# Kernel tuning notes

Measured on AMD Instinct MI355X. Metric: run time of the kernel, lower is better.

## Reference

```python
import jax, jax.numpy as jnp
import numpy as np

B, N, T, H = 32, 16, 64, 256


def setup_inputs() -> dict:
    key = jax.random.key(0)
    k1, k2, k3 = jax.random.split(key, 3)
    node_rnn_output = jax.random.normal(k1, (B, T, H), dtype=jnp.float32)
    neigh_rnn_output = jax.random.normal(k2, (B, N, T, H), dtype=jnp.float32)
    # neighbor counts in [1, N] to avoid divide-by-zero in 1/sqrt scaling
    neighbors_number = jax.random.randint(k3, (B,), 1, N + 1, dtype=jnp.int64)
    return {
        "node_rnn_output": node_rnn_output,
        "neigh_rnn_output": neigh_rnn_output,
        "neighbors_number": neighbors_number,
    }


def reference(node_rnn_output, neigh_rnn_output, neighbors_number):
    b, t, h = node_rnn_output.shape
    n = neigh_rnn_output.shape[1]
    # [B, N*T, H]
    flat_neigh = neigh_rnn_output.reshape(b, n * t, h)
    # repeat node output along time axis: [B, N*T, H]
    stacked_node = jnp.tile(node_rnn_output, (1, n, 1))
    # S = flat_neigh @ stacked_node^T : [B, N*T, N*T]
    S = jnp.einsum("bqh,bkh->bqk", flat_neigh, stacked_node)
    scale = jnp.sqrt(neighbors_number.astype(S.dtype))  # [B]
    S = S / scale[:, None, None]
    A = jax.nn.softmax(S, axis=-1)
    # dropout with p=0 (eval / reference) is identity
    W = A.sum(axis=1).reshape(b, n, t)  # [B, N, T]
    output = jnp.einsum("bqk,bkh->bqh", A, flat_neigh)  # [B, N*T, H]
    return (output, W)
```

## Files before the change

kernel.cpp:

```cpp
#include <hip/hip_runtime.h>

#define Bc  32
#define Nc  16
#define Tc  64
#define Hc  256
#define NTc 1024

typedef unsigned short u16;
using v8s = __attribute__((ext_vector_type(8))) short;
using v4f = __attribute__((ext_vector_type(4))) float;

static __device__ __forceinline__ u16 f2bf(float x) {
    unsigned u = __float_as_uint(x);
    unsigned r = u + 0x7fffu + ((u >> 16) & 1u);
    return (u16)(r >> 16);
}
static __device__ __forceinline__ float bf2f(u16 h) {
    return __uint_as_float(((unsigned)h) << 16);
}

__global__ __launch_bounds__(256) void prep_kernel(const float* __restrict__ neigh,
                                                   const float* __restrict__ node,
                                                   u16* __restrict__ MT,
                                                   u16* __restrict__ NH,
                                                   u16* __restrict__ NL,
                                                   float* __restrict__ Wsum) {
    __shared__ float Ls[64][68];
    int bk = blockIdx.x, tid = threadIdx.x;

    if (bk < 128) {
        int b = bk >> 2, h0 = (bk & 3) << 6;
#pragma unroll
        for (int rep = 0; rep < 4; rep++) {
            int idx = rep * 256 + tid;
            int t = idx >> 4, c4 = idx & 15;
            const float4* p = (const float4*)(neigh + ((size_t)b * Nc * Tc + t) * Hc + h0) + c4;
            float4 a = make_float4(0.f, 0.f, 0.f, 0.f);
#pragma unroll
            for (int i = 0; i < Nc; i++) {
                float4 v = p[(size_t)i * (Tc * Hc / 4)];
                a.x += v.x; a.y += v.y; a.z += v.z; a.w += v.w;
            }
            const float r = 1.0f / 16.0f;
            Ls[t][c4 * 4 + 0] = a.x * r;
            Ls[t][c4 * 4 + 1] = a.y * r;
            Ls[t][c4 * 4 + 2] = a.z * r;
            Ls[t][c4 * 4 + 3] = a.w * r;
        }
        __syncthreads();
#pragma unroll
        for (int rep = 0; rep < 4; rep++) {
            int idx = rep * 256 + tid;
            int h = idx >> 4, t4 = idx & 15;
            ushort4 o;
            o.x = f2bf(Ls[t4 * 4 + 0][h]);
            o.y = f2bf(Ls[t4 * 4 + 1][h]);
            o.z = f2bf(Ls[t4 * 4 + 2][h]);
            o.w = f2bf(Ls[t4 * 4 + 3][h]);
            *(ushort4*)(MT + ((size_t)b * Hc + h0 + h) * Tc + t4 * 4) = o;
        }
    } else {
        int b = bk - 128;
#pragma unroll
        for (int rep = 0; rep < 16; rep++) {
            int idx = rep * 256 + tid;
            int t = idx >> 6, c4 = idx & 63;
            size_t off = ((size_t)b * Tc + t) * Hc + c4 * 4;
            float4 v = *(const float4*)(node + off);
            ushort4 hs, ls;
            hs.x = f2bf(v.x); ls.x = f2bf(v.x - bf2f(hs.x));
            hs.y = f2bf(v.y); ls.y = f2bf(v.y - bf2f(hs.y));
            hs.z = f2bf(v.z); ls.z = f2bf(v.z - bf2f(hs.z));
            hs.w = f2bf(v.w); ls.w = f2bf(v.w - bf2f(hs.w));
            *(ushort4*)(NH + off) = hs;
            *(ushort4*)(NL + off) = ls;
        }
        if (tid < 64) Wsum[b * 64 + tid] = 0.f;
    }
}

__global__ __launch_bounds__(256, 2) void fused_kernel(const float* __restrict__ neigh,
                                                       const u16* __restrict__ NH,
                                                       const u16* __restrict__ NL,
                                                       const int* __restrict__ nbr,
                                                       const u16* __restrict__ MT,
                                                       float* __restrict__ out,
                                                       float* __restrict__ Wsum) {
    __shared__ u16 Ph[64][72];

    int b  = blockIdx.x >> 4;
    int i  = blockIdx.x & 15;
    int q0 = i << 6;

    int tid  = threadIdx.x;
    int w    = tid >> 6;
    int lane = tid & 63;
    int quad = lane >> 4;
    int c    = lane & 15;

    int nb = (nbr[1] == 0) ? nbr[2 * b] : nbr[b];
    float rscale = rsqrtf((float)nb);

    const float* Xg  = neigh + ((size_t)(b * Nc + i) * Tc + w * 16 + c) * Hc;
    const u16*   NHg = NH + (size_t)b * Tc * Hc;
    const u16*   NLg = NL + (size_t)b * Tc * Hc;
    const u16*   MTg = MT + (size_t)b * Hc * Tc;

    v4f acc[4];
#pragma unroll
    for (int nt = 0; nt < 4; nt++)
#pragma unroll
        for (int rg = 0; rg < 4; rg++) acc[nt][rg] = 0.f;

#pragma unroll 2
    for (int k0 = 0; k0 < Hc; k0 += 32) {
        const float4* xp = (const float4*)(Xg + k0) + quad * 2;
        float4 x0 = xp[0];
        float4 x1 = xp[1];
        float xs[8] = {x0.x, x0.y, x0.z, x0.w, x1.x, x1.y, x1.z, x1.w};
        v8s ah, al;
#pragma unroll
        for (int j = 0; j < 8; j++) {
            u16 h = f2bf(xs[j]);
            ah[j] = (short)h;
            al[j] = (short)f2bf(xs[j] - bf2f(h));
        }
        size_t koff = (size_t)k0 + quad * 8;
#pragma unroll
        for (int nt = 0; nt < 4; nt++) {
            size_t roff = (size_t)(nt * 16 + c) * Hc + koff;
            v8s bh = *(const v8s*)(NHg + roff);
            v8s bl = *(const v8s*)(NLg + roff);
            acc[nt] = __builtin_amdgcn_mfma_f32_16x16x32_bf16(ah, bh, acc[nt], 0, 0, 0);
            acc[nt] = __builtin_amdgcn_mfma_f32_16x16x32_bf16(ah, bl, acc[nt], 0, 0, 0);
            acc[nt] = __builtin_amdgcn_mfma_f32_16x16x32_bf16(al, bh, acc[nt], 0, 0, 0);
        }
    }

#pragma unroll
    for (int nt = 0; nt < 4; nt++)
#pragma unroll
        for (int rg = 0; rg < 4; rg++) acc[nt][rg] *= rscale;

#pragma unroll
    for (int rg = 0; rg < 4; rg++) {
        float m = fmaxf(fmaxf(acc[0][rg], acc[1][rg]), fmaxf(acc[2][rg], acc[3][rg]));
#pragma unroll
        for (int d = 1; d < 16; d <<= 1) m = fmaxf(m, __shfl_xor(m, d));
        float e0 = __expf(acc[0][rg] - m);
        float e1 = __expf(acc[1][rg] - m);
        float e2 = __expf(acc[2][rg] - m);
        float e3 = __expf(acc[3][rg] - m);
        float s = e0 + e1 + e2 + e3;
#pragma unroll
        for (int d = 1; d < 16; d <<= 1) s += __shfl_xor(s, d);
        float inv = 1.0f / s;
        acc[0][rg] = e0 * inv; acc[1][rg] = e1 * inv;
        acc[2][rg] = e2 * inv; acc[3][rg] = e3 * inv;
    }

#pragma unroll
    for (int nt = 0; nt < 4; nt++) {
        float cs = acc[nt][0] + acc[nt][1] + acc[nt][2] + acc[nt][3];
        cs += __shfl_xor(cs, 16);
        cs += __shfl_xor(cs, 32);
        if (quad == 0) atomicAdd(&Wsum[b * Tc + nt * 16 + c], cs);
    }

#pragma unroll
    for (int nt = 0; nt < 4; nt++)
#pragma unroll
        for (int rg = 0; rg < 4; rg++)
            Ph[w * 16 + quad * 4 + rg][nt * 16 + c] = f2bf(acc[nt][rg]);

    __syncthreads();

    v8s pa0 = *(const v8s*)&Ph[w * 16 + c][quad * 8];
    v8s pa1 = *(const v8s*)&Ph[w * 16 + c][32 + quad * 8];

    float* ob = out + ((size_t)b * NTc + q0 + w * 16 + quad * 4) * Hc + c;

#pragma unroll 4
    for (int hc = 0; hc < 16; hc++) {
        const u16* mp = MTg + (size_t)(hc * 16 + c) * Tc + quad * 8;
        v8s b0 = *(const v8s*)mp;
        v8s b1 = *(const v8s*)(mp + 32);
        v4f oc;
#pragma unroll
        for (int rg = 0; rg < 4; rg++) oc[rg] = 0.f;
        oc = __builtin_amdgcn_mfma_f32_16x16x32_bf16(pa0, b0, oc, 0, 0, 0);
        oc = __builtin_amdgcn_mfma_f32_16x16x32_bf16(pa1, b1, oc, 0, 0, 0);
#pragma unroll
        for (int rg = 0; rg < 4; rg++)
            ob[(size_t)rg * Hc + hc * 16] = oc[rg];
    }
}

__global__ __launch_bounds__(256) void wexp_kernel(const float* __restrict__ Wsum,
                                                   float* __restrict__ Wout) {
    int idx = blockIdx.x * 256 + threadIdx.x;
    int b = idx >> 10;
    int t = idx & 63;
    Wout[idx] = Wsum[b * Tc + t] * (1.0f / 16.0f);
}

extern "C" void kernel_launch(void* const* d_in, const int* in_sizes, int n_in,
                              void* d_out, int out_size, void* d_ws, size_t ws_size,
                              hipStream_t stream) {
    const float* node  = (const float*)d_in[0];
    const float* neigh = (const float*)d_in[1];
    const int*   nbr   = (const int*)d_in[2];

    float* out = (float*)d_out;

    u16* MTw = (u16*)d_ws;
    u16* NHw = MTw + (size_t)Bc * Hc * Tc;
    u16* NLw = NHw + (size_t)Bc * Tc * Hc;
    float* Ww = (float*)(NLw + (size_t)Bc * Tc * Hc);

    prep_kernel <<<160, 256, 0, stream>>>(neigh, node, MTw, NHw, NLw, Ww);
    fused_kernel<<<512, 256, 0, stream>>>(neigh, NHw, NLw, nbr, MTw, out, Ww);
    wexp_kernel <<<128, 256, 0, stream>>>(Ww, out + (size_t)Bc * NTc * Hc);
}
```

Measured before the change: 120.8 us.

## Stage node operands and MT in swizzled LDS; split prep blocks over time

```diff
diff --git a/kernel.cpp b/kernel.cpp
--- a/kernel.cpp
+++ b/kernel.cpp
@@ -25,16 +25,19 @@
                                                    u16* __restrict__ NH,
                                                    u16* __restrict__ NL,
                                                    float* __restrict__ Wsum) {
-    __shared__ float Ls[64][68];
+    __shared__ float Ls[32][68];
     int bk = blockIdx.x, tid = threadIdx.x;
 
-    if (bk < 128) {
-        int b = bk >> 2, h0 = (bk & 3) << 6;
-#pragma unroll
-        for (int rep = 0; rep < 4; rep++) {
+    if (bk < 256) {
+        int b  = bk >> 3;
+        int sub = bk & 7;
+        int h0 = (sub & 3) << 6;
+        int t0 = (sub >> 2) << 5;
+#pragma unroll
+        for (int rep = 0; rep < 2; rep++) {
             int idx = rep * 256 + tid;
             int t = idx >> 4, c4 = idx & 15;
-            const float4* p = (const float4*)(neigh + ((size_t)b * Nc * Tc + t) * Hc + h0) + c4;
+            const float4* p = (const float4*)(neigh + ((size_t)b * Nc * Tc + t0 + t) * Hc + h0) + c4;
             float4 a = make_float4(0.f, 0.f, 0.f, 0.f);
 #pragma unroll
             for (int i = 0; i < Nc; i++) {
@@ -49,18 +52,18 @@
         }
         __syncthreads();
 #pragma unroll
-        for (int rep = 0; rep < 4; rep++) {
+        for (int rep = 0; rep < 2; rep++) {
             int idx = rep * 256 + tid;
-            int h = idx >> 4, t4 = idx & 15;
+            int h = idx >> 3, t4 = idx & 7;
             ushort4 o;
             o.x = f2bf(Ls[t4 * 4 + 0][h]);
             o.y = f2bf(Ls[t4 * 4 + 1][h]);
             o.z = f2bf(Ls[t4 * 4 + 2][h]);
             o.w = f2bf(Ls[t4 * 4 + 3][h]);
-            *(ushort4*)(MT + ((size_t)b * Hc + h0 + h) * Tc + t4 * 4) = o;
+            *(ushort4*)(MT + ((size_t)b * Hc + h0 + h) * Tc + t0 + t4 * 4) = o;
         }
     } else {
-        int b = bk - 128;
+        int b = bk - 256;
 #pragma unroll
         for (int rep = 0; rep < 16; rep++) {
             int idx = rep * 256 + tid;
@@ -86,6 +89,8 @@
                                                        const u16* __restrict__ MT,
                                                        float* __restrict__ out,
                                                        float* __restrict__ Wsum) {
+    __shared__ u16 NSh[64 * 256];
+    __shared__ u16 NSl[64 * 256];
     __shared__ u16 Ph[64][72];
 
     int b  = blockIdx.x >> 4;
@@ -97,14 +102,25 @@
     int lane = tid & 63;
     int quad = lane >> 4;
     int c    = lane & 15;
+    int r3   = c & 7;
 
     int nb = (nbr[1] == 0) ? nbr[2 * b] : nbr[b];
     float rscale = rsqrtf((float)nb);
 
-    const float* Xg  = neigh + ((size_t)(b * Nc + i) * Tc + w * 16 + c) * Hc;
-    const u16*   NHg = NH + (size_t)b * Tc * Hc;
-    const u16*   NLg = NL + (size_t)b * Tc * Hc;
-    const u16*   MTg = MT + (size_t)b * Hc * Tc;
+    const u16* NHg = NH + (size_t)b * Tc * Hc;
+    const u16* NLg = NL + (size_t)b * Tc * Hc;
+    const u16* MTg = MT + (size_t)b * Hc * Tc;
+    const float* XgL = neigh + ((size_t)(b * Nc + i) * Tc + w * 16 + c) * Hc;
+
+#pragma unroll
+    for (int rep = 0; rep < 8; rep++) {
+        int idx = rep * 256 + tid;
+        int row = idx >> 5, g = idx & 31;
+        int dst = row * 256 + ((g ^ (row & 7)) << 3);
+        *(uint4*)&NSh[dst] = *(const uint4*)(NHg + row * 256 + g * 8);
+        *(uint4*)&NSl[dst] = *(const uint4*)(NLg + row * 256 + g * 8);
+    }
+    __syncthreads();
 
     v4f acc[4];
 #pragma unroll
@@ -114,9 +130,8 @@
 
 #pragma unroll 2
     for (int k0 = 0; k0 < Hc; k0 += 32) {
-        const float4* xp = (const float4*)(Xg + k0) + quad * 2;
-        float4 x0 = xp[0];
-        float4 x1 = xp[1];
+        float4 x0 = *(const float4*)(XgL + k0 + quad * 8);
+        float4 x1 = *(const float4*)(XgL + k0 + quad * 8 + 4);
         float xs[8] = {x0.x, x0.y, x0.z, x0.w, x1.x, x1.y, x1.z, x1.w};
         v8s ah, al;
 #pragma unroll
@@ -125,16 +140,24 @@
             ah[j] = (short)h;
             al[j] = (short)f2bf(xs[j] - bf2f(h));
         }
-        size_t koff = (size_t)k0 + quad * 8;
+        int gk = (k0 >> 3) + quad;
 #pragma unroll
         for (int nt = 0; nt < 4; nt++) {
-            size_t roff = (size_t)(nt * 16 + c) * Hc + koff;
-            v8s bh = *(const v8s*)(NHg + roff);
-            v8s bl = *(const v8s*)(NLg + roff);
+            int off = (nt * 16 + c) * 256 + ((gk ^ r3) << 3);
+            v8s bh = *(const v8s*)&NSh[off];
+            v8s bl = *(const v8s*)&NSl[off];
             acc[nt] = __builtin_amdgcn_mfma_f32_16x16x32_bf16(ah, bh, acc[nt], 0, 0, 0);
             acc[nt] = __builtin_amdgcn_mfma_f32_16x16x32_bf16(ah, bl, acc[nt], 0, 0, 0);
             acc[nt] = __builtin_amdgcn_mfma_f32_16x16x32_bf16(al, bh, acc[nt], 0, 0, 0);
         }
+    }
+
+    uint4 mt[8];
+#pragma unroll
+    for (int rep = 0; rep < 8; rep++) {
+        int idx = rep * 256 + tid;
+        int row = idx >> 3, g = idx & 7;
+        mt[rep] = *(const uint4*)(MTg + row * 64 + g * 8);
     }
 
 #pragma unroll
@@ -175,6 +198,14 @@
 
     __syncthreads();
 
+#pragma unroll
+    for (int rep = 0; rep < 8; rep++) {
+        int idx = rep * 256 + tid;
+        int row = idx >> 3, g = idx & 7;
+        *(uint4*)&NSh[row * 64 + ((g ^ (row & 7)) << 3)] = mt[rep];
+    }
+    __syncthreads();
+
     v8s pa0 = *(const v8s*)&Ph[w * 16 + c][quad * 8];
     v8s pa1 = *(const v8s*)&Ph[w * 16 + c][32 + quad * 8];
 
@@ -182,9 +213,9 @@
 
 #pragma unroll 4
     for (int hc = 0; hc < 16; hc++) {
-        const u16* mp = MTg + (size_t)(hc * 16 + c) * Tc + quad * 8;
-        v8s b0 = *(const v8s*)mp;
-        v8s b1 = *(const v8s*)(mp + 32);
+        int rowm = hc * 16 + c;
+        v8s b0 = *(const v8s*)&NSh[rowm * 64 + ((quad ^ r3) << 3)];
+        v8s b1 = *(const v8s*)&NSh[rowm * 64 + (((4 + quad) ^ r3) << 3)];
         v4f oc;
 #pragma unroll
         for (int rg = 0; rg < 4; rg++) oc[rg] = 0.f;
@@ -218,7 +249,7 @@
     u16* NLw = NHw + (size_t)Bc * Tc * Hc;
     float* Ww = (float*)(NLw + (size_t)Bc * Tc * Hc);
 
-    prep_kernel <<<160, 256, 0, stream>>>(neigh, node, MTw, NHw, NLw, Ww);
+    prep_kernel <<<288, 256, 0, stream>>>(neigh, node, MTw, NHw, NLw, Ww);
     fused_kernel<<<512, 256, 0, stream>>>(neigh, NHw, NLw, nbr, MTw, out, Ww);
     wexp_kernel <<<128, 256, 0, stream>>>(Ww, out + (size_t)Bc * NTc * Hc);
 }
```

Measured after the change: 114.2 us. 5.4% less time.
